# Performance work log

Measured on AMD Instinct MI355X. Metric: run time of the kernel, lower is better.

Reference implementation:

```python
import jax, jax.numpy as jnp
import numpy as np


def _integral(x):
    # x: [C, H, W] -> summed-area table [C, H+1, W+1] with zero first row/col
    s = jnp.cumsum(jnp.cumsum(x, axis=-2), axis=-1)
    return jnp.pad(s, ((0, 0), (1, 0), (1, 0)))


def _box_sums(S, x0, y0, x1, y1):
    # S: [C, H+1, W+1]; boxes half-open [y0:y1, x0:x1] -> sums [C, N]
    return S[:, y1, x1] - S[:, y0, x1] - S[:, y1, x0] + S[:, y0, x0]


def setup_inputs() -> dict:
    key = jax.random.key(0)
    C, H, W, K, N = 256, 512, 512, 21, 2560
    k1, k2, k3, k4, k5, k6, k7 = jax.random.split(key, 7)
    feature_map = jax.random.normal(k1, (C, H, W), dtype=jnp.float32)
    norm_cam_bg = jax.random.uniform(k2, (K, H, W), dtype=jnp.float32)
    # valid crop boxes (xmin, ymin, xmax, ymax) with 8..64 px extent
    x0 = jax.random.randint(k3, (N,), 0, W - 64)
    y0 = jax.random.randint(k4, (N,), 0, H - 64)
    bw = jax.random.randint(k5, (N,), 8, 64)
    bh = jax.random.randint(k6, (N,), 8, 64)
    boxes = jnp.stack([x0, y0, x0 + bw, y0 + bh], axis=1).astype(jnp.int32)
    labels = jax.random.randint(k7, (N,), 0, K).astype(jnp.int32)
    return {"feature_map": feature_map, "norm_cam_bg": norm_cam_bg,
            "boxes": boxes, "labels": labels}


def reference(feature_map, norm_cam_bg, boxes, labels):
    # feature_map: [C, H, W]; norm_cam_bg: [K, H, W]; boxes: [N, 4] int; labels: [N] int
    K = norm_cam_bg.shape[0]
    N = boxes.shape[0]
    x0, y0, x1, y1 = boxes[:, 0], boxes[:, 1], boxes[:, 2], boxes[:, 3]
    area = ((x1 - x0) * (y1 - y0)).astype(feature_map.dtype)  # [N]

    # per-box adaptive_avg_pool2d(region, (1,1)) == mean over region, via integral image
    S = _integral(feature_map)                                # [C, H+1, W+1]
    pool = _box_sums(S, x0, y0, x1, y1).T / area[:, None]     # [N, C]

    # foreground score: fraction of pixels in box where argmax(CAM) == region label
    cam_predict = jnp.argmax(norm_cam_bg, axis=0)             # [H, W]
    onehot = jax.nn.one_hot(cam_predict, K, dtype=feature_map.dtype)  # [H, W, K]
    Sm = _integral(jnp.moveaxis(onehot, -1, 0))               # [K, H+1, W+1]
    fg_sums = _box_sums(Sm, x0, y0, x1, y1)                   # [K, N]
    fg_score = fg_sums[labels, jnp.arange(N)] / area          # [N]

    return pool, fg_score
```

## Files before the change

### kernel.cpp

```cpp
#include <hip/hip_runtime.h>

#define HWD (512*512)
#define Wd 512
#define Hd 512
#define Cd 256
#define Kd 21
#define Nd 2560
#define NSTRIP 4
#define SROWS 128

__device__ __forceinline__ float dpp_scan_incl(float x) {
    int xi, t;
    xi = __float_as_int(x);
    t = __builtin_amdgcn_update_dpp(0, xi, 0x111, 0xf, 0xf, true);
    x += __int_as_float(t);
    xi = __float_as_int(x);
    t = __builtin_amdgcn_update_dpp(0, xi, 0x112, 0xf, 0xf, true);
    x += __int_as_float(t);
    xi = __float_as_int(x);
    t = __builtin_amdgcn_update_dpp(0, xi, 0x114, 0xf, 0xf, true);
    x += __int_as_float(t);
    xi = __float_as_int(x);
    t = __builtin_amdgcn_update_dpp(0, xi, 0x118, 0xf, 0xf, true);
    x += __int_as_float(t);
    xi = __float_as_int(x);
    t = __builtin_amdgcn_update_dpp(0, xi, 0x142, 0xa, 0xf, false);
    x += __int_as_float(t);
    xi = __float_as_int(x);
    t = __builtin_amdgcn_update_dpp(0, xi, 0x143, 0xc, 0xf, false);
    x += __int_as_float(t);
    return x;
}

__global__ __launch_bounds__(512) void k_events(const int* __restrict__ boxes,
                                                int* __restrict__ ev_start,
                                                unsigned int* __restrict__ ev_list) {
    const int t = threadIdx.x;
    __shared__ int cnt[512];
    __shared__ int cur[512];
    __shared__ int tt[8];
    const int lane = t & 63, wv = t >> 6;
    cnt[t] = 0;
    __syncthreads();
    for (int n = t; n < Nd; n += 512) {
        const int y0 = boxes[n * 4 + 1];
        const int y1 = boxes[n * 4 + 3];
        if (y0 > 0) atomicAdd(&cnt[y0 - 1], 1);
        atomicAdd(&cnt[y1 - 1], 1);
    }
    __syncthreads();
    const int v = cnt[t];
    int inc = v;
    #pragma unroll
    for (int d = 1; d < 64; d <<= 1) {
        int u = __shfl_up(inc, d);
        if (lane >= d) inc += u;
    }
    if (lane == 63) tt[wv] = inc;
    __syncthreads();
    int off = 0;
    #pragma unroll
    for (int w = 0; w < 8; ++w) if (w < wv) off += tt[w];
    inc += off;
    cur[t] = inc - v;
    ev_start[t] = inc - v;
    if (t == 511) ev_start[512] = inc;
    __syncthreads();
    for (int n = t; n < Nd; n += 512) {
        const int y0 = boxes[n * 4 + 1];
        const int y1 = boxes[n * 4 + 3];
        if (y0 > 0) {
            const int r = y0 - 1;
            const int p = atomicAdd(&cur[r], 1);
            ev_list[p] = (unsigned)n | ((unsigned)r << 12) | 0x80000000u;
        }
        const int r = y1 - 1;
        const int p = atomicAdd(&cur[r], 1);
        ev_list[p] = (unsigned)n | ((unsigned)r << 12);
    }
}

__global__ __launch_bounds__(512) void k_ipool(const float* __restrict__ f,
                                               const int* __restrict__ boxes,
                                               const int* __restrict__ ev_start,
                                               const unsigned int* __restrict__ ev_list,
                                               float* __restrict__ pool_acc) {
    const int c     = blockIdx.x >> 2;
    const int strip = blockIdx.x & 3;
    const int t = threadIdx.x;
    const int lane = t & 63, wv = t >> 6;
    const float* F = f + (size_t)c * HWD + (size_t)(strip * SROWS) * Wd;

    __shared__ float S[8][512];
    __shared__ float partial[Nd];

    for (int n = t; n < Nd; n += 512) partial[n] = 0.f;

    float colacc = 0.f;

    const float* rp0 = F + (size_t)wv * Wd + lane * 8;
    float4 a0 = *(const float4*)(rp0);
    float4 b0 = *(const float4*)(rp0 + 4);
    const float* rp1 = F + (size_t)(8 + wv) * Wd + lane * 8;
    float4 a1 = *(const float4*)(rp1);
    float4 b1 = *(const float4*)(rp1 + 4);

    for (int yb = 0; yb < SROWS; yb += 8) {
        const bool more2 = (yb + 16 < SROWS);
        float4 na, nb;
        if (more2) {
            const float* np = F + (size_t)(yb + 16 + wv) * Wd + lane * 8;
            na = *(const float4*)(np);
            nb = *(const float4*)(np + 4);
        }

        float v0 = a0.x, v1 = v0 + a0.y, v2 = v1 + a0.z, v3 = v2 + a0.w;
        float v4 = v3 + b0.x, v5 = v4 + b0.y, v6 = v5 + b0.z, v7 = v6 + b0.w;
        const float xx = dpp_scan_incl(v7);
        const float off = xx - v7;
        float4 o0 = { v0 + off, v1 + off, v2 + off, v3 + off };
        float4 o1 = { v4 + off, v5 + off, v6 + off, v7 + off };
        *(float4*)&S[wv][lane * 8]     = o0;
        *(float4*)&S[wv][lane * 8 + 4] = o1;
        __syncthreads();

        float sv[8];
        #pragma unroll
        for (int j = 0; j < 8; ++j) sv[j] = S[j][t];
        #pragma unroll
        for (int j = 0; j < 8; ++j) {
            colacc += sv[j];
            S[j][t] = colacc;
        }
        __syncthreads();

        const int g0 = strip * SROWS + yb;
        const int e0 = ev_start[g0];
        const int e1 = ev_start[g0 + 8];
        for (int e = e0 + t; e < e1; e += 512) {
            const unsigned ev = ev_list[e];
            const int n  = ev & 0xFFF;
            const int rr = (ev >> 12) & 7;
            const int x0 = boxes[n * 4 + 0];
            const int x1 = boxes[n * 4 + 2];
            const float sx1 = S[rr][x1 - 1];
            const float sx0 = (x0 > 0) ? S[rr][x0 - 1] : 0.f;
            const float d = sx1 - sx0;
            partial[n] += (ev & 0x80000000u) ? -d : d;
        }
        __syncthreads();

        a0 = a1; b0 = b1;
        if (more2) { a1 = na; b1 = nb; }
    }

    S[0][t] = colacc;
    __syncthreads();
    for (int n = t; n < Nd; n += 512) {
        const int x0 = boxes[n * 4 + 0];
        const int y0 = boxes[n * 4 + 1];
        const int x1 = boxes[n * 4 + 2];
        const int y1 = boxes[n * 4 + 3];
        float p = partial[n];
        const float tdiff = S[0][x1 - 1] - ((x0 > 0) ? S[0][x0 - 1] : 0.f);
        if (strip < ((y1 - 1) >> 7)) p += tdiff;
        if (y0 > 0 && strip < ((y0 - 1) >> 7)) p -= tdiff;
        pool_acc[((size_t)(strip * Cd + c)) * Nd + n] = p;
    }
}

__global__ __launch_bounds__(512) void k_pool2a(const float* __restrict__ pool_acc,
                                                const float* __restrict__ ncb,
                                                const int* __restrict__ boxes,
                                                float* __restrict__ pool,
                                                unsigned char* __restrict__ map) {
    const int bid = blockIdx.x;
    const int t = threadIdx.x;

    if (bid >= Nd / 32) {
        const int p = (bid - Nd / 32) * 512 + t;
        float best = ncb[p];
        int bi = 0;
        #pragma unroll
        for (int k = 1; k < Kd; ++k) {
            float v = ncb[(size_t)k * HWD + p];
            if (v > best) { best = v; bi = k; }
        }
        map[p] = (unsigned char)bi;
        return;
    }

    __shared__ float P[32][257];
    __shared__ float rarea[32];
    const int n0 = bid * 32;

    if (t < 32) {
        const int x0 = boxes[(n0 + t) * 4 + 0];
        const int y0 = boxes[(n0 + t) * 4 + 1];
        const int x1 = boxes[(n0 + t) * 4 + 2];
        const int y1 = boxes[(n0 + t) * 4 + 3];
        rarea[t] = 1.f / (float)((x1 - x0) * (y1 - y0));
    }

    const int ni = t & 31, ci = t >> 5;
    #pragma unroll
    for (int co = 0; co < 16; ++co) {
        const int c = co * 16 + ci;
        float v = 0.f;
        #pragma unroll
        for (int s = 0; s < NSTRIP; ++s)
            v += pool_acc[((size_t)(s * Cd + c)) * Nd + n0 + ni];
        P[ni][c] = v;
    }
    __syncthreads();

    const int c = t & 255, nn = t >> 8;
    #pragma unroll
    for (int no = 0; no < 16; ++no) {
        const int i = no * 2 + nn;
        pool[(size_t)(n0 + i) * Cd + c] = P[i][c] * rarea[i];
    }
}

__global__ __launch_bounds__(256) void k_fg(const unsigned char* __restrict__ map,
                                            const int* __restrict__ boxes,
                                            const int* __restrict__ labels,
                                            float* __restrict__ fg) {
    const int n = blockIdx.x;
    const int x0 = boxes[n * 4 + 0];
    const int y0 = boxes[n * 4 + 1];
    const int x1 = boxes[n * 4 + 2];
    const int y1 = boxes[n * 4 + 3];
    const int lab = labels[n];
    const int lane = threadIdx.x & 63;
    const int wv   = threadIdx.x >> 6;
    const int w = x1 - x0;

    int cnt = 0;
    for (int yy = y0 + wv; yy < y1; yy += 4) {
        if (lane < w)
            cnt += (map[yy * Wd + x0 + lane] == lab) ? 1 : 0;
    }
    #pragma unroll
    for (int d = 32; d; d >>= 1) cnt += __shfl_down(cnt, d);

    __shared__ int sred[4];
    if (lane == 0) sred[wv] = cnt;
    __syncthreads();
    if (threadIdx.x == 0) {
        int tot = sred[0] + sred[1] + sred[2] + sred[3];
        float area = (float)(w * (y1 - y0));
        fg[n] = (float)tot / area;
    }
}

extern "C" void kernel_launch(void* const* d_in, const int* in_sizes, int n_in,
                              void* d_out, int out_size, void* d_ws, size_t ws_size,
                              hipStream_t stream) {
    (void)in_sizes; (void)n_in; (void)out_size; (void)ws_size;

    const float* feature_map = (const float*)d_in[0];
    const float* norm_cam_bg = (const float*)d_in[1];
    const int*   boxes       = (const int*)d_in[2];
    const int*   labels      = (const int*)d_in[3];

    float* out_pool = (float*)d_out;
    float* out_fg   = out_pool + (size_t)Nd * Cd;

    char* ws = (char*)d_ws;
    unsigned char* map      = (unsigned char*)ws;
    int*           ev_start = (int*)(ws + 262144);
    unsigned int*  ev_list  = (unsigned int*)(ws + 266240);
    float*         pool_acc = (float*)(ws + 286720);

    k_events<<<1, 512, 0, stream>>>(boxes, ev_start, ev_list);
    k_ipool<<<Cd * NSTRIP, 512, 0, stream>>>(feature_map, boxes, ev_start, ev_list,
                                             pool_acc);
    k_pool2a<<<Nd / 32 + 512, 512, 0, stream>>>(pool_acc, norm_cam_bg, boxes,
                                                out_pool, map);
    k_fg<<<Nd, 256, 0, stream>>>(map, boxes, labels, out_fg);
}
```

Baseline: 80.30 us.

## Move CAM argmax into event kernel and fuse fg scoring into pool post kernel

The per-pixel CAM argmax moves out of the pool finalize kernel and into extra blocks of the single-block event-building kernel. It is vectorised to float4 loads and uchar4 stores. The foreground-score kernel is merged into the pool finalize kernel as extra blocks using 8 waves per box, which cuts the launch count from four to three. This lets the argmax overlap the otherwise idle single-block event kernel and removes one launch, though the fg blocks now use 512 threads, which may waste lanes on short boxes.

```diff
diff --git a/kernel.cpp b/kernel.cpp
--- a/kernel.cpp
+++ b/kernel.cpp
@@ -32,10 +32,30 @@
     return x;
 }
 
-__global__ __launch_bounds__(512) void k_events(const int* __restrict__ boxes,
-                                                int* __restrict__ ev_start,
-                                                unsigned int* __restrict__ ev_list) {
+__global__ __launch_bounds__(512) void k_pre(const float* __restrict__ ncb,
+                                             const int* __restrict__ boxes,
+                                             unsigned char* __restrict__ map,
+                                             int* __restrict__ ev_start,
+                                             unsigned int* __restrict__ ev_list) {
     const int t = threadIdx.x;
+    if (blockIdx.x < 128) {
+        const int q = blockIdx.x * 512 + t;
+        float4 best = *(const float4*)(ncb + (size_t)q * 4);
+        int b0 = 0, b1 = 0, b2 = 0, b3 = 0;
+        #pragma unroll
+        for (int k = 1; k < Kd; ++k) {
+            float4 v = *(const float4*)(ncb + (size_t)k * HWD + (size_t)q * 4);
+            if (v.x > best.x) { best.x = v.x; b0 = k; }
+            if (v.y > best.y) { best.y = v.y; b1 = k; }
+            if (v.z > best.z) { best.z = v.z; b2 = k; }
+            if (v.w > best.w) { best.w = v.w; b3 = k; }
+        }
+        uchar4 o = { (unsigned char)b0, (unsigned char)b1,
+                     (unsigned char)b2, (unsigned char)b3 };
+        *(uchar4*)(map + (size_t)q * 4) = o;
+        return;
+    }
+
     __shared__ int cnt[512];
     __shared__ int cur[512];
     __shared__ int tt[8];
@@ -169,31 +189,47 @@
     }
 }
 
-__global__ __launch_bounds__(512) void k_pool2a(const float* __restrict__ pool_acc,
-                                                const float* __restrict__ ncb,
-                                                const int* __restrict__ boxes,
-                                                float* __restrict__ pool,
-                                                unsigned char* __restrict__ map) {
+__global__ __launch_bounds__(512) void k_post(const float* __restrict__ pool_acc,
+                                              const unsigned char* __restrict__ map,
+                                              const int* __restrict__ boxes,
+                                              const int* __restrict__ labels,
+                                              float* __restrict__ pool,
+                                              float* __restrict__ fg) {
     const int bid = blockIdx.x;
     const int t = threadIdx.x;
-
-    if (bid >= Nd / 32) {
-        const int p = (bid - Nd / 32) * 512 + t;
-        float best = ncb[p];
-        int bi = 0;
-        #pragma unroll
-        for (int k = 1; k < Kd; ++k) {
-            float v = ncb[(size_t)k * HWD + p];
-            if (v > best) { best = v; bi = k; }
-        }
-        map[p] = (unsigned char)bi;
-        return;
-    }
-
     __shared__ float P[32][257];
     __shared__ float rarea[32];
+    __shared__ int   sred[8];
+
+    if (bid >= Nd / 32) {
+        const int n = bid - Nd / 32;
+        const int x0 = boxes[n * 4 + 0];
+        const int y0 = boxes[n * 4 + 1];
+        const int x1 = boxes[n * 4 + 2];
+        const int y1 = boxes[n * 4 + 3];
+        const int lab = labels[n];
+        const int lane = t & 63, wv = t >> 6;
+        const int w = x1 - x0;
+
+        int cnt = 0;
+        for (int yy = y0 + wv; yy < y1; yy += 8) {
+            if (lane < w)
+                cnt += (map[yy * Wd + x0 + lane] == lab) ? 1 : 0;
+        }
+        #pragma unroll
+        for (int d = 32; d; d >>= 1) cnt += __shfl_down(cnt, d);
+        if (lane == 0) sred[wv] = cnt;
+        __syncthreads();
+        if (t == 0) {
+            int tot = 0;
+            #pragma unroll
+            for (int i = 0; i < 8; ++i) tot += sred[i];
+            fg[n] = (float)tot / (float)(w * (y1 - y0));
+        }
+        return;
+    }
+
     const int n0 = bid * 32;
-
     if (t < 32) {
         const int x0 = boxes[(n0 + t) * 4 + 0];
         const int y0 = boxes[(n0 + t) * 4 + 1];
@@ -222,38 +258,6 @@
     }
 }
 
-__global__ __launch_bounds__(256) void k_fg(const unsigned char* __restrict__ map,
-                                            const int* __restrict__ boxes,
-                                            const int* __restrict__ labels,
-                                            float* __restrict__ fg) {
-    const int n = blockIdx.x;
-    const int x0 = boxes[n * 4 + 0];
-    const int y0 = boxes[n * 4 + 1];
-    const int x1 = boxes[n * 4 + 2];
-    const int y1 = boxes[n * 4 + 3];
-    const int lab = labels[n];
-    const int lane = threadIdx.x & 63;
-    const int wv   = threadIdx.x >> 6;
-    const int w = x1 - x0;
-
-    int cnt = 0;
-    for (int yy = y0 + wv; yy < y1; yy += 4) {
-        if (lane < w)
-            cnt += (map[yy * Wd + x0 + lane] == lab) ? 1 : 0;
-    }
-    #pragma unroll
-    for (int d = 32; d; d >>= 1) cnt += __shfl_down(cnt, d);
-
-    __shared__ int sred[4];
-    if (lane == 0) sred[wv] = cnt;
-    __syncthreads();
-    if (threadIdx.x == 0) {
-        int tot = sred[0] + sred[1] + sred[2] + sred[3];
-        float area = (float)(w * (y1 - y0));
-        fg[n] = (float)tot / area;
-    }
-}
-
 extern "C" void kernel_launch(void* const* d_in, const int* in_sizes, int n_in,
                               void* d_out, int out_size, void* d_ws, size_t ws_size,
                               hipStream_t stream) {
@@ -273,10 +277,9 @@
     unsigned int*  ev_list  = (unsigned int*)(ws + 266240);
     float*         pool_acc = (float*)(ws + 286720);
 
-    k_events<<<1, 512, 0, stream>>>(boxes, ev_start, ev_list);
+    k_pre<<<129, 512, 0, stream>>>(norm_cam_bg, boxes, map, ev_start, ev_list);
     k_ipool<<<Cd * NSTRIP, 512, 0, stream>>>(feature_map, boxes, ev_start, ev_list,
                                              pool_acc);
-    k_pool2a<<<Nd / 32 + 512, 512, 0, stream>>>(pool_acc, norm_cam_bg, boxes,
-                                                out_pool, map);
-    k_fg<<<Nd, 256, 0, stream>>>(map, boxes, labels, out_fg);
-}
+    k_post<<<Nd / 32 + Nd, 512, 0, stream>>>(pool_acc, map, boxes, labels,
+                                             out_pool, out_fg);
+}
```

Result: faster. 76.75 us, median of 2 (-4.4%).
